# Kernel tuning notes

Measured on AMD Instinct MI355X. Metric: run time of the kernel, lower is better.

Reference implementation:

```python
import jax, jax.numpy as jnp
import numpy as np

N = 50000      # nodes
E = 400000     # edges
D_IN = 128; D_HID = 128; D_OUT = 128
C = 8          # n_channel (== channel_dim)
CNF = 8        # channel_nf
DIM = 3        # spatial dim
EPS = 1e-3     # module eps
BN_EPS = 1e-5


def _pool_matrix(n_channel):
    # RollerPooling: pool_matrix[i] averages a sliding upper-triangular window of size (n-i)
    ones = np.ones((n_channel, n_channel), dtype=np.float32)
    mats = []
    for i in range(n_channel):
        w = n_channel - i
        mats.append((np.triu(ones) - np.triu(ones, k=w)) / w)
    return jnp.asarray(np.stack(mats))  # [C, C, C]


def setup_inputs() -> dict:
    key = jax.random.key(0)
    ks = jax.random.split(key, 20)
    s = 0.02
    src = jax.random.randint(ks[0], (E,), 0, N)
    tgt = jax.random.randint(ks[1], (E,), 0, N)
    rel = jnp.zeros((E,), dtype=src.dtype)  # num_relation = 1
    edge_list = jnp.stack([src, tgt, rel], axis=1)
    inp = {
        "h": jax.random.normal(ks[2], (N, D_IN), jnp.float32),
        "coords": jax.random.normal(ks[3], (N, C, DIM), jnp.float32),
        "channel_attr": jax.random.normal(ks[4], (N, C, CNF), jnp.float32),
        "channel_weights": jax.random.randint(ks[5], (N, C), 0, 3).astype(jnp.float32),
        "edge_weights": jax.random.uniform(ks[6], (E,), jnp.float32),
        "edge_list": edge_list,
        # parameters
        "rl_w": jax.random.normal(ks[7], (CNF * CNF, CNF), jnp.float32) * s,
        "rl_b": jnp.zeros((CNF,), jnp.float32),
        "m_w1": jax.random.normal(ks[8], (2 * D_IN + CNF, D_HID), jnp.float32) * s,
        "m_b1": jnp.zeros((D_HID,), jnp.float32),
        "m_w2": jax.random.normal(ks[9], (D_HID, D_HID), jnp.float32) * s,
        "m_b2": jnp.zeros((D_HID,), jnp.float32),
        "c_w1": jax.random.normal(ks[10], (D_HID, D_HID), jnp.float32) * s,
        "c_b1": jnp.zeros((D_HID,), jnp.float32),
        "c_w2": jax.random.normal(ks[11], (D_HID, C), jnp.float32) * 0.001,  # xavier gain=0.001
        "het_w": jax.random.normal(ks[12], (D_HID, D_OUT), jnp.float32) * s,
        "het_b": jnp.zeros((D_OUT,), jnp.float32),
        "bn_gamma": jnp.ones((D_OUT,), jnp.float32),
        "bn_beta": jnp.zeros((D_OUT,), jnp.float32),
        "w_r": jnp.ones((1,), jnp.float32),
    }
    return inp


def reference(h, coords, channel_attr, channel_weights, edge_weights,
              rl_w, rl_b, m_w1, m_b1, m_w2, m_b2, c_w1, c_b1, c_w2,
              het_w, het_b, bn_gamma, bn_beta, w_r, edge_list):
    silu = jax.nn.silu
    src, tgt, rel = edge_list[:, 0], edge_list[:, 1], edge_list[:, 2]
    n_channel = coords.shape[1]
    num_nodes = h.shape[0]

    # --- radial feature ---
    # pairwise channel distances per edge: [E, C, C]
    diff = coords[tgt][:, :, None, :] - coords[src][:, None, :, :]
    coord_msg = jnp.linalg.norm(diff, axis=-1)
    coord_msg = coord_msg / (jnp.max(coord_msg) + EPS)
    cw = channel_weights
    coord_msg = coord_msg * (cw[tgt][:, :, None] * cw[src][:, None, :])
    # attr_t^T @ msg @ attr_s -> [E, CNF, CNF]
    radial = jnp.einsum('eca,ecd,edb->eab', channel_attr[tgt], coord_msg, channel_attr[src])
    radial = radial.reshape(radial.shape[0], -1)
    radial = radial / (jnp.linalg.norm(radial, axis=-1, keepdims=True) + EPS)
    radial = radial @ rl_w + rl_b  # [E, CNF]

    mask = (cw != 0)
    csum = mask.sum(-1)  # [N]
    pooled_col = (coords[src] * mask[src][:, :, None].astype(coords.dtype)).sum(1)
    pooled_col = pooled_col / (csum[src][:, None].astype(coords.dtype) + EPS)
    coord_diff = coords[tgt] - pooled_col[:, None, :]  # [E, C, DIM]

    # --- message MLP (dropout = identity in eval) ---
    x = jnp.concatenate([h[tgt], h[src], radial], axis=-1)
    m = silu(x @ m_w1 + m_b1)
    m = silu(m @ m_w2 + m_b2)  # [E, hidden]

    # --- coord message with RollerPooling ---
    edge_feat = silu(m @ c_w1 + c_b1) @ c_w2  # [E, C]
    pm = _pool_matrix(n_channel)
    ts = jnp.clip(csum[tgt] - 1, 0, n_channel - 1)
    pooled_edge = jnp.einsum('eij,ej->ei', pm[ts], edge_feat)[..., None]  # [E, C, 1]
    coord_message = coord_diff * pooled_edge  # [E, C, DIM]

    # --- aggregate (scatter to target nodes) ---
    ew = edge_weights[:, None]
    node_agg = jax.ops.segment_sum(m * ew, tgt, num_segments=num_nodes)  # [N, hidden]
    wcm = w_r[rel][:, None, None] * coord_message
    coord_sum = jax.ops.segment_sum(wcm, tgt, num_segments=num_nodes)
    cnt = jax.ops.segment_sum(jnp.ones((wcm.shape[0],), wcm.dtype), tgt, num_segments=num_nodes)
    coord_agg = coord_sum / jnp.clip(cnt, 1.0)[:, None, None]  # mean aggregation

    # --- combine ---
    out = node_agg @ het_w + het_b
    # BatchNorm1d in eval mode with default running stats (mean=0, var=1)
    out = out / jnp.sqrt(1.0 + BN_EPS) * bn_gamma + bn_beta
    out = silu(out)
    node_output = h + out
    coord_output = coords + coord_agg
    return node_output, coord_output
```

## Files before the change

kernel.cpp:

```cpp
#include <hip/hip_runtime.h>

#define NN 50000
#define NE 400000
#define D 128
#define KXP 288
#define KXR 264
#define XSTR 296
#define MSTR 136
#define EPSV 1e-3f

typedef unsigned short u16;
typedef unsigned int u32;
typedef __attribute__((ext_vector_type(4))) float f32x4;
typedef __attribute__((ext_vector_type(8))) short short8;
typedef __attribute__((ext_vector_type(8))) unsigned short ushort8;

__device__ __forceinline__ u16 f2b(float f){
  u32 u = __float_as_uint(f);
  u32 r = u + 0x7fffu + ((u >> 16) & 1u);
  return (u16)(r >> 16);
}
__device__ __forceinline__ float b2f(u16 s){ return __uint_as_float(((u32)s) << 16); }
__device__ __forceinline__ float silu_f(float x){ return x / (1.f + expf(-x)); }

__global__ void k_prep_h(const float* __restrict__ h, u16* __restrict__ hbf){
  int i = blockIdx.x * 256 + threadIdx.x;
  if (i < NN * D) hbf[i] = f2b(h[i]);
}

__global__ void k_prep_w(const float* __restrict__ m_w1, const float* __restrict__ m_w2,
                         const float* __restrict__ c_w1, const float* __restrict__ het_w,
                         u16* __restrict__ W1t, u16* __restrict__ W2t,
                         u16* __restrict__ C1t, u16* __restrict__ HtT){
  int i = blockIdx.x * 256 + threadIdx.x;
  if (i < D * KXP){
    int c = i / KXP, k = i - c * KXP;
    W1t[i] = f2b(k < KXR ? m_w1[k * D + c] : 0.f);
    return;
  }
  i -= D * KXP;
  if (i < D * D){ int c = i >> 7, k = i & 127; W2t[i] = f2b(m_w2[k * D + c]); return; }
  i -= D * D;
  if (i < D * D){ int c = i >> 7, k = i & 127; C1t[i] = f2b(c_w1[k * D + c]); return; }
  i -= D * D;
  if (i < D * D){ int c = i >> 7, k = i & 127; HtT[i] = f2b(het_w[k * D + c]); return; }
}

__global__ void k_node_pre(const float* __restrict__ coords, const float* __restrict__ cw,
                           float* __restrict__ pooled, int* __restrict__ tsn){
  int n = blockIdx.x * 256 + threadIdx.x;
  if (n >= NN) return;
  int cs = 0; float px = 0.f, py = 0.f, pz = 0.f;
  #pragma unroll
  for (int c = 0; c < 8; c++){
    float w = cw[n * 8 + c];
    if (w != 0.f){
      cs++;
      px += coords[(size_t)n * 24 + c * 3 + 0];
      py += coords[(size_t)n * 24 + c * 3 + 1];
      pz += coords[(size_t)n * 24 + c * 3 + 2];
    }
  }
  float inv = 1.f / ((float)cs + EPSV);
  pooled[n * 3 + 0] = px * inv;
  pooled[n * 3 + 1] = py * inv;
  pooled[n * 3 + 2] = pz * inv;
  int ts = cs - 1; ts = ts < 0 ? 0 : (ts > 7 ? 7 : ts);
  tsn[n] = ts;
}

__global__ __launch_bounds__(256) void k_edge_max(const float* __restrict__ coords,
                                                  const int* __restrict__ el,
                                                  u32* __restrict__ maxsq, u32* __restrict__ cnt){
  int e = blockIdx.x * 256 + threadIdx.x;
  float vm = 0.f;
  if (e < NE){
    int s = el[e * 3 + 0], t = el[e * 3 + 1];
    float ct[24], cs_[24];
    #pragma unroll
    for (int i = 0; i < 24; i++) ct[i] = coords[(size_t)t * 24 + i];
    #pragma unroll
    for (int i = 0; i < 24; i++) cs_[i] = coords[(size_t)s * 24 + i];
    #pragma unroll
    for (int c1 = 0; c1 < 8; c1++){
      #pragma unroll
      for (int c2 = 0; c2 < 8; c2++){
        float dx = ct[c1 * 3 + 0] - cs_[c2 * 3 + 0];
        float dy = ct[c1 * 3 + 1] - cs_[c2 * 3 + 1];
        float dz = ct[c1 * 3 + 2] - cs_[c2 * 3 + 2];
        vm = fmaxf(vm, dx * dx + dy * dy + dz * dz);
      }
    }
    atomicAdd(&cnt[t], 1u);
  }
  __shared__ float red[256];
  red[threadIdx.x] = vm;
  __syncthreads();
  for (int s2 = 128; s2 > 0; s2 >>= 1){
    if (threadIdx.x < s2) red[threadIdx.x] = fmaxf(red[threadIdx.x], red[threadIdx.x + s2]);
    __syncthreads();
  }
  if (threadIdx.x == 0) atomicMax(maxsq, __float_as_uint(red[0]));
}

__global__ __launch_bounds__(256) void k_radial(const float* __restrict__ coords,
                                                const float* __restrict__ attr,
                                                const float* __restrict__ cw,
                                                const int* __restrict__ el,
                                                const float* __restrict__ rl_w,
                                                const float* __restrict__ rl_b,
                                                const u32* __restrict__ maxsq,
                                                float* __restrict__ radial8){
  __shared__ float sct[64][24], scs[64][24], sAs[64][64], scwt[64][8], scws[64][8], stmp[64][64];
  const int tid = threadIdx.x;
  const int er = tid >> 2;
  const int q = tid & 3;
  const int e = blockIdx.x * 64 + er;
  const int s = el[e * 3 + 0];
  const int t = el[e * 3 + 1];

  #pragma unroll
  for (int i = 0; i < 6; i++) sct[er][q * 6 + i] = coords[(size_t)t * 24 + q * 6 + i];
  #pragma unroll
  for (int i = 0; i < 6; i++) scs[er][q * 6 + i] = coords[(size_t)s * 24 + q * 6 + i];
  #pragma unroll
  for (int i = 0; i < 16; i++) sAs[er][q * 16 + i] = attr[(size_t)s * 64 + q * 16 + i];
  #pragma unroll
  for (int i = 0; i < 2; i++){
    scwt[er][q * 2 + i] = cw[(size_t)t * 8 + q * 2 + i];
    scws[er][q * 2 + i] = cw[(size_t)s * 8 + q * 2 + i];
  }
  __syncthreads();

  const float scale = 1.f / (sqrtf(__uint_as_float(*maxsq)) + EPSV);

  float tmp[2][8];
  #pragma unroll
  for (int ci = 0; ci < 2; ci++)
    #pragma unroll
    for (int b = 0; b < 8; b++) tmp[ci][b] = 0.f;
  #pragma unroll
  for (int d = 0; d < 8; d++){
    float as[8];
    #pragma unroll
    for (int b = 0; b < 8; b++) as[b] = sAs[er][d * 8 + b];
    #pragma unroll
    for (int ci = 0; ci < 2; ci++){
      int c = q * 2 + ci;
      float dx = sct[er][c * 3 + 0] - scs[er][d * 3 + 0];
      float dy = sct[er][c * 3 + 1] - scs[er][d * 3 + 1];
      float dz = sct[er][c * 3 + 2] - scs[er][d * 3 + 2];
      float msg = sqrtf(dx * dx + dy * dy + dz * dz) * scale * scwt[er][c] * scws[er][d];
      #pragma unroll
      for (int b = 0; b < 8; b++) tmp[ci][b] += msg * as[b];
    }
  }
  #pragma unroll
  for (int ci = 0; ci < 2; ci++)
    #pragma unroll
    for (int b = 0; b < 8; b++) stmp[er][(q * 2 + ci) * 8 + b] = tmp[ci][b];
  __syncthreads();

  float rad[2][8];
  #pragma unroll
  for (int ai = 0; ai < 2; ai++)
    #pragma unroll
    for (int b = 0; b < 8; b++) rad[ai][b] = 0.f;
  #pragma unroll
  for (int c = 0; c < 8; c++){
    float at0 = attr[(size_t)t * 64 + c * 8 + 2 * q + 0];
    float at1 = attr[(size_t)t * 64 + c * 8 + 2 * q + 1];
    #pragma unroll
    for (int b = 0; b < 8; b++){
      float tv = stmp[er][c * 8 + b];
      rad[0][b] += at0 * tv;
      rad[1][b] += at1 * tv;
    }
  }
  float sq = 0.f;
  #pragma unroll
  for (int ai = 0; ai < 2; ai++)
    #pragma unroll
    for (int b = 0; b < 8; b++) sq += rad[ai][b] * rad[ai][b];
  sq += __shfl_xor(sq, 1);
  sq += __shfl_xor(sq, 2);
  const float rn = 1.f / (sqrtf(sq) + EPSV);

  float o[8];
  #pragma unroll
  for (int j = 0; j < 8; j++) o[j] = 0.f;
  #pragma unroll
  for (int ai = 0; ai < 2; ai++){
    int a = 2 * q + ai;
    #pragma unroll
    for (int b = 0; b < 8; b++){
      float v = rad[ai][b] * rn;
      int row = a * 8 + b;
      #pragma unroll
      for (int j = 0; j < 8; j++) o[j] += v * rl_w[row * 8 + j];
    }
  }
  #pragma unroll
  for (int j = 0; j < 8; j++){
    o[j] += __shfl_xor(o[j], 1);
    o[j] += __shfl_xor(o[j], 2);
  }
  if (q == 0){
    #pragma unroll
    for (int j = 0; j < 8; j++) radial8[(size_t)e * 8 + j] = o[j] + rl_b[j];
  }
}

__global__ __launch_bounds__(256, 2) void k_edge_mlp(
    const int* __restrict__ el, const float* __restrict__ ewg,
    const float* __restrict__ radial8, const u16* __restrict__ hbf,
    const u16* __restrict__ W1t, const u16* __restrict__ W2t, const u16* __restrict__ C1t,
    const float* __restrict__ m_b1, const float* __restrict__ m_b2,
    const float* __restrict__ c_b1, const float* __restrict__ c_w2,
    const float* __restrict__ coords, const float* __restrict__ pooled,
    const int* __restrict__ tsn, const float* __restrict__ w_r,
    float* __restrict__ out_node, float* __restrict__ out_coord)
{
  __shared__ u16 sx[64 * XSTR];
  __shared__ u16 sm[64 * MSTR];
  __shared__ float sef[64 * 8];
  __shared__ int s_tgt[64];
  __shared__ int s_src[64];
  __shared__ float s_ew[64];

  const int tid = threadIdx.x;
  const int lane = tid & 63;
  const int wv = tid >> 6;
  const int wrow = wv * 16;
  const int e0 = blockIdx.x * 64;
  const int lc = lane & 15;
  const int lk = (lane >> 4) * 8;
  const f32x4 zero = {0.f, 0.f, 0.f, 0.f};

  {
    const int er = wrow + (lane >> 2);
    const int q = lane & 3;
    const int e = e0 + er;
    const int s = el[e * 3 + 0];
    const int t = el[e * 3 + 1];
    if (q == 0){ s_src[er] = s; s_tgt[er] = t; s_ew[er] = ewg[e]; }
    const u16* srow = (q < 2) ? (hbf + (size_t)t * D + q * 64)
                              : (hbf + (size_t)s * D + (q - 2) * 64);
    const int colbase = (q < 2) ? (q * 64) : (128 + (q - 2) * 64);
    u16* dst = sx + er * XSTR + colbase;
    #pragma unroll
    for (int i = 0; i < 8; i++)
      *(ushort8*)(dst + i * 8) = *(const ushort8*)(srow + i * 8);
    if (q == 0){
      #pragma unroll
      for (int j = 0; j < 8; j++) sx[er * XSTR + 256 + j] = f2b(radial8[(size_t)e * 8 + j]);
      #pragma unroll
      for (int j = 264; j < 288; j++) sx[er * XSTR + j] = 0;
    }
  }
  __syncthreads();

  f32x4 acc[8];

  #pragma unroll
  for (int nb = 0; nb < 8; nb++) acc[nb] = zero;
  #pragma unroll
  for (int kb = 0; kb < 9; kb++){
    short8 a = *(const short8*)(sx + (wrow + lc) * XSTR + kb * 32 + lk);
    #pragma unroll
    for (int nb = 0; nb < 8; nb++){
      short8 b = *(const short8*)(W1t + (size_t)(nb * 16 + lc) * KXP + kb * 32 + lk);
      acc[nb] = __builtin_amdgcn_mfma_f32_16x16x32_bf16(a, b, acc[nb], 0, 0, 0);
    }
  }
  #pragma unroll
  for (int nb = 0; nb < 8; nb++){
    const int col = nb * 16 + lc;
    const float bias = m_b1[col];
    #pragma unroll
    for (int j = 0; j < 4; j++){
      const int row = wrow + (lane >> 4) * 4 + j;
      sm[row * MSTR + col] = f2b(silu_f(acc[nb][j] + bias));
    }
  }

  #pragma unroll
  for (int nb = 0; nb < 8; nb++) acc[nb] = zero;
  #pragma unroll
  for (int kb = 0; kb < 4; kb++){
    short8 a = *(const short8*)(sm + (wrow + lc) * MSTR + kb * 32 + lk);
    #pragma unroll
    for (int nb = 0; nb < 8; nb++){
      short8 b = *(const short8*)(W2t + (size_t)(nb * 16 + lc) * D + kb * 32 + lk);
      acc[nb] = __builtin_amdgcn_mfma_f32_16x16x32_bf16(a, b, acc[nb], 0, 0, 0);
    }
  }
  #pragma unroll
  for (int nb = 0; nb < 8; nb++){
    const int col = nb * 16 + lc;
    const float bias = m_b2[col];
    #pragma unroll
    for (int j = 0; j < 4; j++){
      const int row = wrow + (lane >> 4) * 4 + j;
      const float v = silu_f(acc[nb][j] + bias);
      atomicAdd(&out_node[(size_t)s_tgt[row] * D + col], v * s_ew[row]);
      sm[row * MSTR + col] = f2b(v);
    }
  }

  #pragma unroll
  for (int nb = 0; nb < 8; nb++) acc[nb] = zero;
  #pragma unroll
  for (int kb = 0; kb < 4; kb++){
    short8 a = *(const short8*)(sm + (wrow + lc) * MSTR + kb * 32 + lk);
    #pragma unroll
    for (int nb = 0; nb < 8; nb++){
      short8 b = *(const short8*)(C1t + (size_t)(nb * 16 + lc) * D + kb * 32 + lk);
      acc[nb] = __builtin_amdgcn_mfma_f32_16x16x32_bf16(a, b, acc[nb], 0, 0, 0);
    }
  }
  #pragma unroll
  for (int nb = 0; nb < 8; nb++){
    const int col = nb * 16 + lc;
    const float bias = c_b1[col];
    #pragma unroll
    for (int j = 0; j < 4; j++){
      const int row = wrow + (lane >> 4) * 4 + j;
      sx[row * XSTR + col] = f2b(silu_f(acc[nb][j] + bias));
    }
  }

  {
    const int r0 = wrow + (lane >> 3);
    const int c8 = lane & 7;
    float a0 = 0.f, a1 = 0.f;
    #pragma unroll
    for (int kk = 0; kk < 128; kk += 8){
      ushort8 v0 = *(const ushort8*)(sx + r0 * XSTR + kk);
      ushort8 v1 = *(const ushort8*)(sx + (r0 + 8) * XSTR + kk);
      #pragma unroll
      for (int j = 0; j < 8; j++){
        const float wv2 = c_w2[(kk + j) * 8 + c8];
        a0 += b2f((u16)v0[j]) * wv2;
        a1 += b2f((u16)v1[j]) * wv2;
      }
    }
    sef[r0 * 8 + c8] = a0;
    sef[(r0 + 8) * 8 + c8] = a1;
  }

  {
    const int er = wrow + (lane >> 2);
    const int q = lane & 3;
    const int t = s_tgt[er], s = s_src[er];
    const int ts = tsn[t];
    const int w8 = 8 - ts;
    const float invw = 1.f / (float)w8;
    const float wr0 = w_r[0];
    const float p0 = pooled[s * 3 + 0], p1 = pooled[s * 3 + 1], p2 = pooled[s * 3 + 2];
    #pragma unroll
    for (int ci = 0; ci < 2; ci++){
      const int c = q * 2 + ci;
      float pe = 0.f;
      const int hi = (c + w8 < 8) ? (c + w8) : 8;
      for (int j = c; j < hi; j++) pe += sef[er * 8 + j];
      pe *= invw * wr0;
      const size_t ob = (size_t)t * 24 + c * 3;
      atomicAdd(&out_coord[ob + 0], (coords[(size_t)t * 24 + c * 3 + 0] - p0) * pe);
      atomicAdd(&out_coord[ob + 1], (coords[(size_t)t * 24 + c * 3 + 1] - p1) * pe);
      atomicAdd(&out_coord[ob + 2], (coords[(size_t)t * 24 + c * 3 + 2] - p2) * pe);
    }
  }
}

__global__ __launch_bounds__(256) void k_final(
    const float* __restrict__ h, const float* __restrict__ coords,
    const u16* __restrict__ HtT, const float* __restrict__ het_b,
    const float* __restrict__ bn_g, const float* __restrict__ bn_b,
    const u32* __restrict__ cnt, float* __restrict__ dout)
{
  __shared__ u16 sa[64 * MSTR];
  const int tid = threadIdx.x, lane = tid & 63, wv = tid >> 6, wrow = wv * 16;
  const int nb0 = blockIdx.x * 64;
  float* out_node = dout;
  float* out_coord = dout + (size_t)NN * D;
  const int lc = lane & 15, lk = (lane >> 4) * 8;
  const f32x4 zero = {0.f, 0.f, 0.f, 0.f};

  #pragma unroll
  for (int i = 0; i < 32; i++){
    const int idx = i * 64 + lane;
    const int r = idx >> 7, c = idx & 127;
    sa[(wrow + r) * MSTR + c] = f2b(out_node[(size_t)(nb0 + wrow + r) * D + c]);
  }

  f32x4 acc[8];
  #pragma unroll
  for (int nb = 0; nb < 8; nb++) acc[nb] = zero;
  #pragma unroll
  for (int kb = 0; kb < 4; kb++){
    short8 a = *(const short8*)(sa + (wrow + lc) * MSTR + kb * 32 + lk);
    #pragma unroll
    for (int nb = 0; nb < 8; nb++){
      short8 b = *(const short8*)(HtT + (size_t)(nb * 16 + lc) * D + kb * 32 + lk);
      acc[nb] = __builtin_amdgcn_mfma_f32_16x16x32_bf16(a, b, acc[nb], 0, 0, 0);
    }
  }
  const float invs = rsqrtf(1.f + 1e-5f);
  #pragma unroll
  for (int nb = 0; nb < 8; nb++){
    const int col = nb * 16 + lc;
    const float hb = het_b[col], g = bn_g[col], be = bn_b[col];
    #pragma unroll
    for (int j = 0; j < 4; j++){
      const int row = wrow + (lane >> 4) * 4 + j;
      const int node = nb0 + row;
      if (node < NN){
        float v = silu_f((acc[nb][j] + hb) * invs * g + be);
        out_node[(size_t)node * D + col] = v + h[(size_t)node * D + col];
      }
    }
  }
  #pragma unroll
  for (int i = 0; i < 6; i++){
    const int idx = i * 256 + tid;
    const int nl = idx / 24, rem = idx - nl * 24;
    const int node = nb0 + nl;
    if (node < NN){
      const size_t o = (size_t)node * 24 + rem;
      const u32 cn = cnt[node];
      const float cv = (float)(cn > 0u ? cn : 1u);
      out_coord[o] = coords[o] + out_coord[o] / cv;
    }
  }
}

extern "C" void kernel_launch(void* const* d_in, const int* in_sizes, int n_in,
                              void* d_out, int out_size, void* d_ws, size_t ws_size,
                              hipStream_t stream)
{
  const float* h      = (const float*)d_in[0];
  const float* coords = (const float*)d_in[1];
  const float* cattr  = (const float*)d_in[2];
  const float* cw     = (const float*)d_in[3];
  const float* ewg    = (const float*)d_in[4];
  const int*   el     = (const int*)  d_in[5];
  const float* rl_w   = (const float*)d_in[6];
  const float* rl_b   = (const float*)d_in[7];
  const float* m_w1   = (const float*)d_in[8];
  const float* m_b1   = (const float*)d_in[9];
  const float* m_w2   = (const float*)d_in[10];
  const float* m_b2   = (const float*)d_in[11];
  const float* c_w1   = (const float*)d_in[12];
  const float* c_b1   = (const float*)d_in[13];
  const float* c_w2   = (const float*)d_in[14];
  const float* het_w  = (const float*)d_in[15];
  const float* het_b  = (const float*)d_in[16];
  const float* bn_g   = (const float*)d_in[17];
  const float* bn_b   = (const float*)d_in[18];
  const float* w_r    = (const float*)d_in[19];

  char* wsb = (char*)d_ws;
  size_t off = 0;
  auto take = [&](size_t bytes)->char*{
    char* p = wsb + off;
    off = (off + bytes + 255) & ~(size_t)255;
    return p;
  };
  u32*   maxsq  = (u32*)  take(4);
  float* pooled = (float*)take((size_t)NN * 3 * 4);
  int*   tsn    = (int*)  take((size_t)NN * 4);
  u32*   cnt    = (u32*)  take((size_t)NN * 4);
  float* rad8   = (float*)take((size_t)NE * 8 * 4);
  u16*   hbf    = (u16*)  take((size_t)NN * D * 2);
  u16*   W1t    = (u16*)  take((size_t)D * KXP * 2);
  u16*   W2t    = (u16*)  take((size_t)D * D * 2);
  u16*   C1t    = (u16*)  take((size_t)D * D * 2);
  u16*   HtT    = (u16*)  take((size_t)D * D * 2);

  float* out_node  = (float*)d_out;
  float* out_coord = out_node + (size_t)NN * D;

  hipMemsetAsync(d_out, 0, (size_t)out_size * sizeof(float), stream);
  hipMemsetAsync(maxsq, 0, 4, stream);
  hipMemsetAsync(cnt, 0, (size_t)NN * 4, stream);

  k_prep_h  <<<dim3((NN * D) / 256), dim3(256), 0, stream>>>(h, hbf);
  k_prep_w  <<<dim3((D * KXP + 3 * D * D) / 256), dim3(256), 0, stream>>>(m_w1, m_w2, c_w1, het_w, W1t, W2t, C1t, HtT);
  k_node_pre<<<dim3((NN + 255) / 256), dim3(256), 0, stream>>>(coords, cw, pooled, tsn);
  k_edge_max<<<dim3((NE + 255) / 256), dim3(256), 0, stream>>>(coords, el, maxsq, cnt);
  k_radial  <<<dim3(NE / 64), dim3(256), 0, stream>>>(coords, cattr, cw, el, rl_w, rl_b, maxsq, rad8);
  k_edge_mlp<<<dim3(NE / 64), dim3(256), 0, stream>>>(el, ewg, rad8, hbf, W1t, W2t, C1t,
        m_b1, m_b2, c_b1, c_w2, coords, pooled, tsn, w_r, out_node, out_coord);
  k_final   <<<dim3((NN + 63) / 64), dim3(256), 0, stream>>>(h, coords, HtT, het_b, bn_g, bn_b, cnt, (float*)d_out);
}
```

Measured before the change: 879.0 us.

## Reuse LDS buffer, use hardware float atomics, MFMA final projection, raise occupancy

Drops the separate sm shared buffer and stores the intermediate activations in spare column ranges of sx. This cuts LDS use per block, so launch bounds are raised to allow 4 blocks per CU. The block-level barrier after the gather is removed, since each wave only touches its own 16 rows. The scalar c_w2 matvec is replaced with one MFMA against a zero-padded bf16 transposed weight, which adds bf16 rounding to that projection. Float atomics now go through unsafeAtomicAdd to get hardware fp32 atomics instead of a possible CAS loop, and the higher occupancy target risks register spills.

New measurement: 918.9 us. 4.5% more time.

```diff
diff --git a/kernel.cpp b/kernel.cpp
--- a/kernel.cpp
+++ b/kernel.cpp
@@ -6,7 +6,6 @@
 #define KXP 288
 #define KXR 264
 #define XSTR 296
-#define MSTR 136
 #define EPSV 1e-3f
 
 typedef unsigned short u16;
@@ -22,6 +21,7 @@
 }
 __device__ __forceinline__ float b2f(u16 s){ return __uint_as_float(((u32)s) << 16); }
 __device__ __forceinline__ float silu_f(float x){ return x / (1.f + expf(-x)); }
+__device__ __forceinline__ void atomAddF(float* p, float v){ unsafeAtomicAdd(p, v); }
 
 __global__ void k_prep_h(const float* __restrict__ h, u16* __restrict__ hbf){
   int i = blockIdx.x * 256 + threadIdx.x;
@@ -30,8 +30,10 @@
 
 __global__ void k_prep_w(const float* __restrict__ m_w1, const float* __restrict__ m_w2,
                          const float* __restrict__ c_w1, const float* __restrict__ het_w,
+                         const float* __restrict__ c_w2,
                          u16* __restrict__ W1t, u16* __restrict__ W2t,
-                         u16* __restrict__ C1t, u16* __restrict__ HtT){
+                         u16* __restrict__ C1t, u16* __restrict__ HtT,
+                         u16* __restrict__ C2t){
   int i = blockIdx.x * 256 + threadIdx.x;
   if (i < D * KXP){
     int c = i / KXP, k = i - c * KXP;
@@ -44,6 +46,8 @@
   if (i < D * D){ int c = i >> 7, k = i & 127; C1t[i] = f2b(c_w1[k * D + c]); return; }
   i -= D * D;
   if (i < D * D){ int c = i >> 7, k = i & 127; HtT[i] = f2b(het_w[k * D + c]); return; }
+  i -= D * D;
+  if (i < 16 * D){ int n = i >> 7, k = i & 127; C2t[i] = f2b(n < 8 ? c_w2[k * 8 + n] : 0.f); return; }
 }
 
 __global__ void k_node_pre(const float* __restrict__ coords, const float* __restrict__ cw,
@@ -211,18 +215,18 @@
   }
 }
 
-__global__ __launch_bounds__(256, 2) void k_edge_mlp(
+__global__ __launch_bounds__(256, 4) void k_edge_mlp(
     const int* __restrict__ el, const float* __restrict__ ewg,
     const float* __restrict__ radial8, const u16* __restrict__ hbf,
     const u16* __restrict__ W1t, const u16* __restrict__ W2t, const u16* __restrict__ C1t,
+    const u16* __restrict__ C2t,
     const float* __restrict__ m_b1, const float* __restrict__ m_b2,
-    const float* __restrict__ c_b1, const float* __restrict__ c_w2,
+    const float* __restrict__ c_b1,
     const float* __restrict__ coords, const float* __restrict__ pooled,
     const int* __restrict__ tsn, const float* __restrict__ w_r,
     float* __restrict__ out_node, float* __restrict__ out_coord)
 {
   __shared__ u16 sx[64 * XSTR];
-  __shared__ u16 sm[64 * MSTR];
   __shared__ float sef[64 * 8];
   __shared__ int s_tgt[64];
   __shared__ int s_src[64];
@@ -258,7 +262,6 @@
       for (int j = 264; j < 288; j++) sx[er * XSTR + j] = 0;
     }
   }
-  __syncthreads();
 
   f32x4 acc[8];
 
@@ -280,7 +283,7 @@
     #pragma unroll
     for (int j = 0; j < 4; j++){
       const int row = wrow + (lane >> 4) * 4 + j;
-      sm[row * MSTR + col] = f2b(silu_f(acc[nb][j] + bias));
+      sx[row * XSTR + col] = f2b(silu_f(acc[nb][j] + bias));
     }
   }
 
@@ -288,7 +291,7 @@
   for (int nb = 0; nb < 8; nb++) acc[nb] = zero;
   #pragma unroll
   for (int kb = 0; kb < 4; kb++){
-    short8 a = *(const short8*)(sm + (wrow + lc) * MSTR + kb * 32 + lk);
+    short8 a = *(const short8*)(sx + (wrow + lc) * XSTR + kb * 32 + lk);
     #pragma unroll
     for (int nb = 0; nb < 8; nb++){
       short8 b = *(const short8*)(W2t + (size_t)(nb * 16 + lc) * D + kb * 32 + lk);
@@ -303,8 +306,8 @@
     for (int j = 0; j < 4; j++){
       const int row = wrow + (lane >> 4) * 4 + j;
       const float v = silu_f(acc[nb][j] + bias);
-      atomicAdd(&out_node[(size_t)s_tgt[row] * D + col], v * s_ew[row]);
-      sm[row * MSTR + col] = f2b(v);
+      atomAddF(&out_node[(size_t)s_tgt[row] * D + col], v * s_ew[row]);
+      sx[row * XSTR + 128 + col] = f2b(v);
     }
   }
 
@@ -312,7 +315,7 @@
   for (int nb = 0; nb < 8; nb++) acc[nb] = zero;
   #pragma unroll
   for (int kb = 0; kb < 4; kb++){
-    short8 a = *(const short8*)(sm + (wrow + lc) * MSTR + kb * 32 + lk);
+    short8 a = *(const short8*)(sx + (wrow + lc) * XSTR + 128 + kb * 32 + lk);
     #pragma unroll
     for (int nb = 0; nb < 8; nb++){
       short8 b = *(const short8*)(C1t + (size_t)(nb * 16 + lc) * D + kb * 32 + lk);
@@ -331,22 +334,20 @@
   }
 
   {
-    const int r0 = wrow + (lane >> 3);
-    const int c8 = lane & 7;
-    float a0 = 0.f, a1 = 0.f;
-    #pragma unroll
-    for (int kk = 0; kk < 128; kk += 8){
-      ushort8 v0 = *(const ushort8*)(sx + r0 * XSTR + kk);
-      ushort8 v1 = *(const ushort8*)(sx + (r0 + 8) * XSTR + kk);
+    f32x4 a4 = zero;
+    #pragma unroll
+    for (int kb = 0; kb < 4; kb++){
+      short8 a = *(const short8*)(sx + (wrow + lc) * XSTR + kb * 32 + lk);
+      short8 b = *(const short8*)(C2t + (size_t)lc * D + kb * 32 + lk);
+      a4 = __builtin_amdgcn_mfma_f32_16x16x32_bf16(a, b, a4, 0, 0, 0);
+    }
+    if (lc < 8){
       #pragma unroll
-      for (int j = 0; j < 8; j++){
-        const float wv2 = c_w2[(kk + j) * 8 + c8];
-        a0 += b2f((u16)v0[j]) * wv2;
-        a1 += b2f((u16)v1[j]) * wv2;
+      for (int j = 0; j < 4; j++){
+        const int row = wrow + (lane >> 4) * 4 + j;
+        sef[row * 8 + lc] = a4[j];
       }
     }
-    sef[r0 * 8 + c8] = a0;
-    sef[(r0 + 8) * 8 + c8] = a1;
   }
 
   {
@@ -366,13 +367,14 @@
       for (int j = c; j < hi; j++) pe += sef[er * 8 + j];
       pe *= invw * wr0;
       const size_t ob = (size_t)t * 24 + c * 3;
-      atomicAdd(&out_coord[ob + 0], (coords[(size_t)t * 24 + c * 3 + 0] - p0) * pe);
-      atomicAdd(&out_coord[ob + 1], (coords[(size_t)t * 24 + c * 3 + 1] - p1) * pe);
-      atomicAdd(&out_coord[ob + 2], (coords[(size_t)t * 24 + c * 3 + 2] - p2) * pe);
-    }
-  }
-}
-
+      atomAddF(&out_coord[ob + 0], (coords[(size_t)t * 24 + c * 3 + 0] - p0) * pe);
+      atomAddF(&out_coord[ob + 1], (coords[(size_t)t * 24 + c * 3 + 1] - p1) * pe);
+      atomAddF(&out_coord[ob + 2], (coords[(size_t)t * 24 + c * 3 + 2] - p2) * pe);
+    }
+  }
+}
+
+#define MSTR 136
 __global__ __launch_bounds__(256) void k_final(
     const float* __restrict__ h, const float* __restrict__ coords,
     const u16* __restrict__ HtT, const float* __restrict__ het_b,
@@ -477,6 +479,7 @@
   u16*   W2t    = (u16*)  take((size_t)D * D * 2);
   u16*   C1t    = (u16*)  take((size_t)D * D * 2);
   u16*   HtT    = (u16*)  take((size_t)D * D * 2);
+  u16*   C2t    = (u16*)  take((size_t)16 * D * 2);
 
   float* out_node  = (float*)d_out;
   float* out_coord = out_node + (size_t)NN * D;
@@ -486,11 +489,12 @@
   hipMemsetAsync(cnt, 0, (size_t)NN * 4, stream);
 
   k_prep_h  <<<dim3((NN * D) / 256), dim3(256), 0, stream>>>(h, hbf);
-  k_prep_w  <<<dim3((D * KXP + 3 * D * D) / 256), dim3(256), 0, stream>>>(m_w1, m_w2, c_w1, het_w, W1t, W2t, C1t, HtT);
+  k_prep_w  <<<dim3((D * KXP + 3 * D * D + 16 * D) / 256), dim3(256), 0, stream>>>(
+        m_w1, m_w2, c_w1, het_w, c_w2, W1t, W2t, C1t, HtT, C2t);
   k_node_pre<<<dim3((NN + 255) / 256), dim3(256), 0, stream>>>(coords, cw, pooled, tsn);
   k_edge_max<<<dim3((NE + 255) / 256), dim3(256), 0, stream>>>(coords, el, maxsq, cnt);
   k_radial  <<<dim3(NE / 64), dim3(256), 0, stream>>>(coords, cattr, cw, el, rl_w, rl_b, maxsq, rad8);
-  k_edge_mlp<<<dim3(NE / 64), dim3(256), 0, stream>>>(el, ewg, rad8, hbf, W1t, W2t, C1t,
-        m_b1, m_b2, c_b1, c_w2, coords, pooled, tsn, w_r, out_node, out_coord);
+  k_edge_mlp<<<dim3(NE / 64), dim3(256), 0, stream>>>(el, ewg, rad8, hbf, W1t, W2t, C1t, C2t,
+        m_b1, m_b2, c_b1, coords, pooled, tsn, w_r, out_node, out_coord);
   k_final   <<<dim3((NN + 63) / 64), dim3(256), 0, stream>>>(h, coords, HtT, het_b, bn_g, bn_b, cnt, (float*)d_out);
 }
```
